# Optimization experiments

Hardware: AMD Instinct MI355X
Metric: run time of the kernel (lower is better)

The kernel has to match this reference:

```python
import jax, jax.numpy as jnp
import numpy as np

N = 100000      # nodes
E = 1600000     # nnz of precomputed A^K (avg degree 16)
D = 64          # in_feats
C = 64          # n_classes
LN_EPS = 1e-5


def setup_inputs() -> dict:
    key = jax.random.key(0)
    ks = jax.random.split(key, 8)
    feat = jax.random.normal(ks[0], (N, D), dtype=jnp.float32)
    feat_ori = jax.random.normal(ks[1], (N, D), dtype=jnp.float32)
    row = jax.random.randint(ks[2], (E,), 0, N)
    col = jax.random.randint(ks[3], (E,), 0, N)
    adj_vals = jax.random.uniform(ks[4], (E,), dtype=jnp.float32)
    # Linear params (xavier_uniform weight, zero bias)
    limit = float(np.sqrt(6.0 / (D + C)))
    W = jax.random.uniform(ks[5], (C, D), dtype=jnp.float32, minval=-limit, maxval=limit)
    b = jnp.zeros((C,), dtype=jnp.float32)
    # LayerNorm params
    gamma = jnp.ones((C,), dtype=jnp.float32)
    beta = jnp.zeros((C,), dtype=jnp.float32)
    return {"feat": feat, "feat_ori": feat_ori, "row": row, "col": col,
            "adj_vals": adj_vals, "W": W, "b": b, "gamma": gamma, "beta": beta}


def reference(feat, feat_ori, row, col, adj_vals, W, b, gamma, beta):
    # NOTE: in the source, h = (1-alpha)*feat + alpha*feat_ori is dead code
    # (immediately overwritten by the SpMM of raw feat), so it is omitted.
    # SpMM: h[i] = sum_{e: row[e]=i} adj_vals[e] * feat[col[e]]   -> [N, D]
    msgs = adj_vals[:, None] * feat[col]            # [E, D] gather + scale
    h = jax.ops.segment_sum(msgs, row, num_segments=N)  # [N, D] scatter-add
    # Dense Linear: [N, D] @ [D, C] + [C]
    h = jnp.einsum('nd,cd->nc', h, W) + b
    # LayerNorm over last dim
    mu = jnp.mean(h, axis=-1, keepdims=True)
    var = jnp.mean(jnp.square(h - mu), axis=-1, keepdims=True)
    h = (h - mu) * jax.lax.rsqrt(var + LN_EPS) * gamma + beta
    return h
```

## Files before the change

### kernel.cpp

```cpp
#include <hip/hip_runtime.h>


typedef unsigned int u32;
typedef unsigned short u16;
typedef unsigned long long u64;
#define RFL(x) __builtin_amdgcn_readfirstlane(x)

#define NBLKC 64
#define MAXBK 2048
#define CAP 1280

__device__ __forceinline__ float bf2f(u16 v) {
    return __uint_as_float((u32)v << 16);
}
__device__ __forceinline__ u16 f2bf(float f) {
    u32 b = __float_as_uint(f);
    return (u16)((b + 0x7FFFu + ((b >> 16) & 1u)) >> 16);
}

__global__ __launch_bounds__(256) void k_bhist(const int* __restrict__ row,
                                               u32* __restrict__ hist2d,
                                               int E, int NBK, int CH) {
    __shared__ u32 cnt[MAXBK];
    int tid = threadIdx.x;
    for (int i = tid; i < NBK; i += 256) cnt[i] = 0;
    __syncthreads();
    int e0 = blockIdx.x * CH;
    int e1 = e0 + CH; if (e1 > E) e1 = E;
    int ev = e1 & ~3;
    for (int i = e0 + tid * 4; i < ev; i += 1024) {
        int4 r = *reinterpret_cast<const int4*>(&row[i]);
        atomicAdd(&cnt[(u32)r.x >> 6], 1u);
        atomicAdd(&cnt[(u32)r.y >> 6], 1u);
        atomicAdd(&cnt[(u32)r.z >> 6], 1u);
        atomicAdd(&cnt[(u32)r.w >> 6], 1u);
    }
    { int i = ev + tid; if (i < e1) atomicAdd(&cnt[(u32)row[i] >> 6], 1u); }
    __syncthreads();
    u32* dst = hist2d + (size_t)blockIdx.x * NBK;
    for (int i = tid; i < NBK; i += 256) dst[i] = cnt[i];
}

__device__ __forceinline__ u32 blk_scan256(u32 v, u32* wsum, u32& total) {
    int lane = threadIdx.x & 63, wid = threadIdx.x >> 6;
    u32 incl = v;
#pragma unroll
    for (int o = 1; o < 64; o <<= 1) {
        u32 u = __shfl_up(incl, o);
        if (lane >= o) incl += u;
    }
    if (lane == 63) wsum[wid] = incl;
    __syncthreads();
    u32 woff = 0;
    for (int w = 0; w < wid; ++w) woff += wsum[w];
    total = wsum[0] + wsum[1] + wsum[2] + wsum[3];
    __syncthreads();
    return woff + incl - v;
}

__global__ __launch_bounds__(256) void k_bscan(u32* __restrict__ hist2d,
                                               u32* __restrict__ btot,
                                               int NBLK, int NBK) {
    __shared__ u32 wsum[4];
    int bkt = blockIdx.x;
    u32 carry = 0;
    for (int r = 0; r < NBLK; r += 256) {
        int blk = r + threadIdx.x;
        u32 v = (blk < NBLK) ? hist2d[(size_t)blk * NBK + bkt] : 0;
        u32 tot;
        u32 ex = blk_scan256(v, wsum, tot);
        if (blk < NBLK) hist2d[(size_t)blk * NBK + bkt] = ex + carry;
        carry += tot;
    }
    if (threadIdx.x == 0) btot[bkt] = carry;
}

__global__ __launch_bounds__(256) void k_scanb2(const u32* __restrict__ btot,
                                                u32* __restrict__ bbase,
                                                int NBK, int E) {
    __shared__ u32 wsum[4];
    u32 carry = 0;
    for (int r = 0; r < NBK; r += 256) {
        int i = r + threadIdx.x;
        u32 v = (i < NBK) ? btot[i] : 0;
        u32 tot;
        u32 ex = blk_scan256(v, wsum, tot);
        if (i < NBK) bbase[i] = ex + carry;
        carry += tot;
    }
    if (threadIdx.x == 0) bbase[NBK] = (u32)E;
}

__global__ __launch_bounds__(256) void k_scatgemm(
    const int* __restrict__ row, const int* __restrict__ col,
    const float* __restrict__ vals, const u32* __restrict__ hist2d,
    const u32* __restrict__ bbase, u64* __restrict__ epair1,
    const float* __restrict__ feat, const float* __restrict__ W,
    u16* __restrict__ G, int E, int N, int NBK, int NBLK, int CH)
{
    __shared__ __align__(16) u32 smem[4096];
    int tid = threadIdx.x;
    if ((int)blockIdx.x < NBLK) {
        u32* lbase = smem;
        u32* lcnt  = smem + NBK;
        int blk = blockIdx.x;
        const u32* hrow = hist2d + (size_t)blk * NBK;
        for (int i = tid; i < NBK; i += 256) {
            lbase[i] = bbase[i] + hrow[i];
            lcnt[i] = 0;
        }
        __syncthreads();
        int e0 = blk * CH;
        int e1 = e0 + CH; if (e1 > E) e1 = E;
        int ev = e1 & ~3;
        for (int i = e0 + tid * 4; i < ev; i += 1024) {
            int4 r = *reinterpret_cast<const int4*>(&row[i]);
            int4 c = *reinterpret_cast<const int4*>(&col[i]);
            float4 v = *reinterpret_cast<const float4*>(&vals[i]);
            u32 k0 = (u32)r.x >> 6, k1 = (u32)r.y >> 6;
            u32 k2 = (u32)r.z >> 6, k3 = (u32)r.w >> 6;
            u32 q0 = atomicAdd(&lcnt[k0], 1u);
            u32 q1 = atomicAdd(&lcnt[k1], 1u);
            u32 q2 = atomicAdd(&lcnt[k2], 1u);
            u32 q3 = atomicAdd(&lcnt[k3], 1u);
            epair1[lbase[k0] + q0] = (u64)((u32)c.x | (((u32)r.x & 63u) << 26))
                                   | ((u64)__float_as_uint(v.x) << 32);
            epair1[lbase[k1] + q1] = (u64)((u32)c.y | (((u32)r.y & 63u) << 26))
                                   | ((u64)__float_as_uint(v.y) << 32);
            epair1[lbase[k2] + q2] = (u64)((u32)c.z | (((u32)r.z & 63u) << 26))
                                   | ((u64)__float_as_uint(v.z) << 32);
            epair1[lbase[k3] + q3] = (u64)((u32)c.w | (((u32)r.w & 63u) << 26))
                                   | ((u64)__float_as_uint(v.w) << 32);
        }
        {
            int i = ev + tid;
            if (i < e1) {
                u32 r = (u32)row[i];
                u32 k = r >> 6;
                u32 q = atomicAdd(&lcnt[k], 1u);
                epair1[lbase[k] + q] = (u64)((u32)col[i] | ((r & 63u) << 26))
                                     | ((u64)__float_as_uint(vals[i]) << 32);
            }
        }
    } else {
        float* fs = (float*)smem;
        int lane = tid & 63, wid = tid >> 6;
        int n0 = ((int)blockIdx.x - NBLK) * 64;
        int valid = N - n0; if (valid > 64) valid = 64;
        int elems = valid * 64;
        for (int idx = tid * 4; idx < elems; idx += 1024)
            *reinterpret_cast<float4*>(&fs[idx]) =
                *reinterpret_cast<const float4*>(&feat[(size_t)n0 * 64 + idx]);
        float wr[64];
#pragma unroll
        for (int d4 = 0; d4 < 16; ++d4) {
            float4 w4 = *reinterpret_cast<const float4*>(&W[lane * 64 + d4 * 4]);
            wr[d4 * 4 + 0] = w4.x; wr[d4 * 4 + 1] = w4.y;
            wr[d4 * 4 + 2] = w4.z; wr[d4 * 4 + 3] = w4.w;
        }
        __syncthreads();
        for (int j = 0; j < 16; ++j) {
            int r = wid * 16 + j;
            if (r >= valid) break;
            float oa[4] = {0.f, 0.f, 0.f, 0.f};
#pragma unroll
            for (int d4 = 0; d4 < 16; ++d4) {
                float4 h4 = *reinterpret_cast<const float4*>(&fs[r * 64 + d4 * 4]);
                oa[d4 & 3] = fmaf(h4.x, wr[d4 * 4 + 0],
                            fmaf(h4.y, wr[d4 * 4 + 1],
                            fmaf(h4.z, wr[d4 * 4 + 2],
                            fmaf(h4.w, wr[d4 * 4 + 3], oa[d4 & 3]))));
            }
            G[(size_t)(n0 + r) * 64 + lane] = f2bf((oa[0] + oa[1]) + (oa[2] + oa[3]));
        }
    }
}

__global__ __launch_bounds__(256) void k_node2(
    const u16* __restrict__ G, const u64* __restrict__ epair1,
    const u32* __restrict__ bbase, const float* __restrict__ bias,
    const float* __restrict__ gamma, const float* __restrict__ beta,
    float* __restrict__ out, int N)
{
    __shared__ u64 sp[CAP];
    __shared__ u32 cnt[64], base[64], cnt2[32];
    int tid = threadIdx.x, lane = tid & 63, wid = tid >> 6;
    int bkt  = blockIdx.x >> 1;
    int half = blockIdx.x & 1;
    if (tid < 64) cnt[tid] = 0;
    if (tid < 32) cnt2[tid] = 0;
    __syncthreads();
    int s = RFL((int)bbase[bkt]);
    int t = RFL((int)bbase[bkt + 1]);

    const u32* meta1 = (const u32*)epair1;
    for (int i = s + tid; i < t; i += 256)
        atomicAdd(&cnt[meta1[2 * (size_t)i] >> 26], 1u);
    __syncthreads();
    if (tid < 64) {
        u32 v = cnt[tid];
        u32 incl = v;
#pragma unroll
        for (int o = 1; o < 64; o <<= 1) {
            u32 u = __shfl_up(incl, o);
            if (tid >= o) incl += u;
        }
        base[tid] = incl - v;
    }
    __syncthreads();
    int r0 = half << 5;
    int myoff = base[r0];
    int myend = (half ? (t - s) : base[32]);
    int myedges = myend - myoff;
    bool fits = (myedges <= CAP);

    if (fits) {
        for (int i = s + tid; i < t; i += 256) {
            u64 p = epair1[i];
            u32 mm = (u32)p;
            u32 r = mm >> 26;
            if ((int)(r >> 5) == half) {
                u32 rank = atomicAdd(&cnt2[r & 31u], 1u);
                sp[base[r] - myoff + rank] =
                    (p & 0xFFFFFFFF00000000ull) | (u64)(mm & 0x03FFFFFFu);
            }
        }
    }
    __syncthreads();

    int rbase = (bkt << 6) + r0;
    for (int j = 0; j < 8; ++j) {
        int rr = (wid << 3) + j;
        int r = r0 + rr;
        int n = rbase + rr;
        if (n >= N) break;
        float acc0 = 0.f, acc1 = 0.f;
        if (fits) {
            int e0 = base[r] - myoff, e1 = e0 + cnt[r];
            int i = e0;
            for (; i + 8 <= e1; i += 8) {
                u64 p0 = sp[i],     p1 = sp[i + 1];
                u64 p2 = sp[i + 2], p3 = sp[i + 3];
                u64 p4 = sp[i + 4], p5 = sp[i + 5];
                u64 p6 = sp[i + 6], p7 = sp[i + 7];
                u32 c0 = RFL((u32)p0), b0 = RFL((u32)(p0 >> 32));
                u32 c1 = RFL((u32)p1), b1 = RFL((u32)(p1 >> 32));
                u32 c2 = RFL((u32)p2), b2 = RFL((u32)(p2 >> 32));
                u32 c3 = RFL((u32)p3), b3 = RFL((u32)(p3 >> 32));
                u32 c4 = RFL((u32)p4), b4 = RFL((u32)(p4 >> 32));
                u32 c5 = RFL((u32)p5), b5 = RFL((u32)(p5 >> 32));
                u32 c6 = RFL((u32)p6), b6 = RFL((u32)(p6 >> 32));
                u32 c7 = RFL((u32)p7), b7 = RFL((u32)(p7 >> 32));
                float g0 = bf2f(G[((size_t)c0 << 6) | lane]);
                float g1 = bf2f(G[((size_t)c1 << 6) | lane]);
                float g2 = bf2f(G[((size_t)c2 << 6) | lane]);
                float g3 = bf2f(G[((size_t)c3 << 6) | lane]);
                float g4 = bf2f(G[((size_t)c4 << 6) | lane]);
                float g5 = bf2f(G[((size_t)c5 << 6) | lane]);
                float g6 = bf2f(G[((size_t)c6 << 6) | lane]);
                float g7 = bf2f(G[((size_t)c7 << 6) | lane]);
                acc0 = fmaf(__uint_as_float(b0), g0, acc0);
                acc1 = fmaf(__uint_as_float(b1), g1, acc1);
                acc0 = fmaf(__uint_as_float(b2), g2, acc0);
                acc1 = fmaf(__uint_as_float(b3), g3, acc1);
                acc0 = fmaf(__uint_as_float(b4), g4, acc0);
                acc1 = fmaf(__uint_as_float(b5), g5, acc1);
                acc0 = fmaf(__uint_as_float(b6), g6, acc0);
                acc1 = fmaf(__uint_as_float(b7), g7, acc1);
            }
            for (; i < e1; ++i) {
                u64 p = sp[i];
                u32 c = RFL((u32)p), b = RFL((u32)(p >> 32));
                acc0 = fmaf(__uint_as_float(b), bf2f(G[((size_t)c << 6) | lane]), acc0);
            }
        } else {
            for (int i = s; i < t; ++i) {
                u64 p = epair1[i];
                u32 mm = RFL((u32)p);
                if ((int)(mm >> 26) == r) {
                    u32 b = RFL((u32)(p >> 32));
                    acc0 = fmaf(__uint_as_float(b),
                                bf2f(G[((size_t)(mm & 0x03FFFFFFu) << 6) | lane]), acc0);
                }
            }
        }
        float o = acc0 + acc1 + bias[lane];

        float ssum = o;
#pragma unroll
        for (int off = 32; off; off >>= 1) ssum += __shfl_xor(ssum, off);
        float mu = ssum * 0.015625f;
        float dv = o - mu;
        float vs = dv * dv;
#pragma unroll
        for (int off = 32; off; off >>= 1) vs += __shfl_xor(vs, off);
        float inv = rsqrtf(vs * 0.015625f + 1e-5f);
        out[((size_t)n << 6) + lane] = dv * inv * gamma[lane] + beta[lane];
    }
}

extern "C" void kernel_launch(void* const* d_in, const int* in_sizes, int n_in,
                              void* d_out, int out_size, void* d_ws, size_t ws_size,
                              hipStream_t stream) {
    const float* feat  = (const float*)d_in[0];
    const int*   row   = (const int*)d_in[2];
    const int*   col   = (const int*)d_in[3];
    const float* vals  = (const float*)d_in[4];
    const float* W     = (const float*)d_in[5];
    const float* bias  = (const float*)d_in[6];
    const float* gamma = (const float*)d_in[7];
    const float* beta  = (const float*)d_in[8];
    float* out = (float*)d_out;

    const int D = 64;
    int N = in_sizes[0] / D;
    int E = in_sizes[2];

    int NBK  = (N + 63) / 64;
    int NBLK = NBLKC;
    int CH   = (((E + NBLK - 1) / NBLK) + 3) & ~3;
    int NG   = (N + 63) / 64;

    char* ws = (char*)d_ws;
    u16*   G      = (u16*)ws;
    size_t off1   = (((size_t)N * 128) + 255) & ~(size_t)255;
    u64*   epair1 = (u64*)(ws + off1);
    size_t off2   = off1 + (((size_t)E * 8 + 255) & ~(size_t)255);
    u32*   hist2d = (u32*)(ws + off2);
    size_t off3   = off2 + (((size_t)NBLK * NBK * 4 + 255) & ~(size_t)255);
    u32*   btot   = (u32*)(ws + off3);
    u32*   bbase  = btot + NBK;

    k_bhist   <<<NBLK, 256, 0, stream>>>(row, hist2d, E, NBK, CH);
    k_bscan   <<<NBK, 256, 0, stream>>>(hist2d, btot, NBLK, NBK);
    k_scanb2  <<<1, 256, 0, stream>>>(btot, bbase, NBK, E);
    k_scatgemm<<<NBLK + NG, 256, 0, stream>>>(row, col, vals, hist2d, bbase,
                                              epair1, feat, W, G,
                                              E, N, NBK, NBLK, CH);
    k_node2   <<<NBK * 2, 256, 0, stream>>>(G, epair1, bbase, bias, gamma,
                                            beta, out, N);
}
```

Before: 134.2 us.

## Split fused scatter/GEMM kernel and widen scatter to 128 blocks of 1024 threads

Splits the combined scatter+GEMM kernel into a dedicated bucket-scatter kernel and a separate feature-transform GEMM kernel, launched back to back. The edge chunk count doubles to 128, and each scatter block now runs 1024 threads, so many more waves place edges into buckets. This targets the scatter phase, which ran on only 64 blocks of 256 threads. In exchange it adds a kernel launch, serializes the GEMM after the scatter instead of overlapping them in one grid, and doubles the histogram/scan work over blocks.

Result: slower. 143.4 us (+6.8%).

```diff
diff --git a/kernel.cpp b/kernel.cpp
--- a/kernel.cpp
+++ b/kernel.cpp
@@ -6,7 +6,7 @@
 typedef unsigned long long u64;
 #define RFL(x) __builtin_amdgcn_readfirstlane(x)
 
-#define NBLKC 64
+#define NBLKC 128
 #define MAXBK 2048
 #define CAP 1280
 
@@ -91,88 +91,88 @@
     if (threadIdx.x == 0) bbase[NBK] = (u32)E;
 }
 
-__global__ __launch_bounds__(256) void k_scatgemm(
+__global__ __launch_bounds__(1024) void k_scat(
     const int* __restrict__ row, const int* __restrict__ col,
     const float* __restrict__ vals, const u32* __restrict__ hist2d,
     const u32* __restrict__ bbase, u64* __restrict__ epair1,
-    const float* __restrict__ feat, const float* __restrict__ W,
-    u16* __restrict__ G, int E, int N, int NBK, int NBLK, int CH)
+    int E, int NBK, int CH)
 {
-    __shared__ __align__(16) u32 smem[4096];
+    __shared__ u32 lbase[MAXBK];
+    __shared__ u32 lcnt[MAXBK];
     int tid = threadIdx.x;
-    if ((int)blockIdx.x < NBLK) {
-        u32* lbase = smem;
-        u32* lcnt  = smem + NBK;
-        int blk = blockIdx.x;
-        const u32* hrow = hist2d + (size_t)blk * NBK;
-        for (int i = tid; i < NBK; i += 256) {
-            lbase[i] = bbase[i] + hrow[i];
-            lcnt[i] = 0;
-        }
-        __syncthreads();
-        int e0 = blk * CH;
-        int e1 = e0 + CH; if (e1 > E) e1 = E;
-        int ev = e1 & ~3;
-        for (int i = e0 + tid * 4; i < ev; i += 1024) {
-            int4 r = *reinterpret_cast<const int4*>(&row[i]);
-            int4 c = *reinterpret_cast<const int4*>(&col[i]);
-            float4 v = *reinterpret_cast<const float4*>(&vals[i]);
-            u32 k0 = (u32)r.x >> 6, k1 = (u32)r.y >> 6;
-            u32 k2 = (u32)r.z >> 6, k3 = (u32)r.w >> 6;
-            u32 q0 = atomicAdd(&lcnt[k0], 1u);
-            u32 q1 = atomicAdd(&lcnt[k1], 1u);
-            u32 q2 = atomicAdd(&lcnt[k2], 1u);
-            u32 q3 = atomicAdd(&lcnt[k3], 1u);
-            epair1[lbase[k0] + q0] = (u64)((u32)c.x | (((u32)r.x & 63u) << 26))
-                                   | ((u64)__float_as_uint(v.x) << 32);
-            epair1[lbase[k1] + q1] = (u64)((u32)c.y | (((u32)r.y & 63u) << 26))
-                                   | ((u64)__float_as_uint(v.y) << 32);
-            epair1[lbase[k2] + q2] = (u64)((u32)c.z | (((u32)r.z & 63u) << 26))
-                                   | ((u64)__float_as_uint(v.z) << 32);
-            epair1[lbase[k3] + q3] = (u64)((u32)c.w | (((u32)r.w & 63u) << 26))
-                                   | ((u64)__float_as_uint(v.w) << 32);
-        }
-        {
-            int i = ev + tid;
-            if (i < e1) {
-                u32 r = (u32)row[i];
-                u32 k = r >> 6;
-                u32 q = atomicAdd(&lcnt[k], 1u);
-                epair1[lbase[k] + q] = (u64)((u32)col[i] | ((r & 63u) << 26))
-                                     | ((u64)__float_as_uint(vals[i]) << 32);
-            }
-        }
-    } else {
-        float* fs = (float*)smem;
-        int lane = tid & 63, wid = tid >> 6;
-        int n0 = ((int)blockIdx.x - NBLK) * 64;
-        int valid = N - n0; if (valid > 64) valid = 64;
-        int elems = valid * 64;
-        for (int idx = tid * 4; idx < elems; idx += 1024)
-            *reinterpret_cast<float4*>(&fs[idx]) =
-                *reinterpret_cast<const float4*>(&feat[(size_t)n0 * 64 + idx]);
-        float wr[64];
+    int blk = blockIdx.x;
+    const u32* hrow = hist2d + (size_t)blk * NBK;
+    for (int i = tid; i < NBK; i += 1024) {
+        lbase[i] = bbase[i] + hrow[i];
+        lcnt[i] = 0;
+    }
+    __syncthreads();
+    int e0 = blk * CH;
+    int e1 = e0 + CH; if (e1 > E) e1 = E;
+    int ev = e1 & ~3;
+    for (int i = e0 + tid * 4; i < ev; i += 4096) {
+        int4 r = *reinterpret_cast<const int4*>(&row[i]);
+        int4 c = *reinterpret_cast<const int4*>(&col[i]);
+        float4 v = *reinterpret_cast<const float4*>(&vals[i]);
+        u32 k0 = (u32)r.x >> 6, k1 = (u32)r.y >> 6;
+        u32 k2 = (u32)r.z >> 6, k3 = (u32)r.w >> 6;
+        u32 q0 = atomicAdd(&lcnt[k0], 1u);
+        u32 q1 = atomicAdd(&lcnt[k1], 1u);
+        u32 q2 = atomicAdd(&lcnt[k2], 1u);
+        u32 q3 = atomicAdd(&lcnt[k3], 1u);
+        epair1[lbase[k0] + q0] = (u64)((u32)c.x | (((u32)r.x & 63u) << 26))
+                               | ((u64)__float_as_uint(v.x) << 32);
+        epair1[lbase[k1] + q1] = (u64)((u32)c.y | (((u32)r.y & 63u) << 26))
+                               | ((u64)__float_as_uint(v.y) << 32);
+        epair1[lbase[k2] + q2] = (u64)((u32)c.z | (((u32)r.z & 63u) << 26))
+                               | ((u64)__float_as_uint(v.z) << 32);
+        epair1[lbase[k3] + q3] = (u64)((u32)c.w | (((u32)r.w & 63u) << 26))
+                               | ((u64)__float_as_uint(v.w) << 32);
+    }
+    {
+        int i = ev + tid;
+        if (i < e1) {
+            u32 r = (u32)row[i];
+            u32 k = r >> 6;
+            u32 q = atomicAdd(&lcnt[k], 1u);
+            epair1[lbase[k] + q] = (u64)((u32)col[i] | ((r & 63u) << 26))
+                                 | ((u64)__float_as_uint(vals[i]) << 32);
+        }
+    }
+}
+
+__global__ __launch_bounds__(256) void k_gemm(const float* __restrict__ feat,
+                                              const float* __restrict__ W,
+                                              u16* __restrict__ G, int N) {
+    __shared__ float fs[4096];
+    int lane = threadIdx.x & 63, wid = threadIdx.x >> 6;
+    int n0 = blockIdx.x * 64;
+    int valid = N - n0; if (valid > 64) valid = 64;
+    int elems = valid * 64;
+    for (int idx = threadIdx.x * 4; idx < elems; idx += 1024)
+        *reinterpret_cast<float4*>(&fs[idx]) =
+            *reinterpret_cast<const float4*>(&feat[(size_t)n0 * 64 + idx]);
+    float wr[64];
+#pragma unroll
+    for (int d4 = 0; d4 < 16; ++d4) {
+        float4 w4 = *reinterpret_cast<const float4*>(&W[lane * 64 + d4 * 4]);
+        wr[d4 * 4 + 0] = w4.x; wr[d4 * 4 + 1] = w4.y;
+        wr[d4 * 4 + 2] = w4.z; wr[d4 * 4 + 3] = w4.w;
+    }
+    __syncthreads();
+    for (int j = 0; j < 16; ++j) {
+        int r = wid * 16 + j;
+        if (r >= valid) break;
+        float oa[4] = {0.f, 0.f, 0.f, 0.f};
 #pragma unroll
         for (int d4 = 0; d4 < 16; ++d4) {
-            float4 w4 = *reinterpret_cast<const float4*>(&W[lane * 64 + d4 * 4]);
-            wr[d4 * 4 + 0] = w4.x; wr[d4 * 4 + 1] = w4.y;
-            wr[d4 * 4 + 2] = w4.z; wr[d4 * 4 + 3] = w4.w;
-        }
-        __syncthreads();
-        for (int j = 0; j < 16; ++j) {
-            int r = wid * 16 + j;
-            if (r >= valid) break;
-            float oa[4] = {0.f, 0.f, 0.f, 0.f};
-#pragma unroll
-            for (int d4 = 0; d4 < 16; ++d4) {
-                float4 h4 = *reinterpret_cast<const float4*>(&fs[r * 64 + d4 * 4]);
-                oa[d4 & 3] = fmaf(h4.x, wr[d4 * 4 + 0],
-                            fmaf(h4.y, wr[d4 * 4 + 1],
-                            fmaf(h4.z, wr[d4 * 4 + 2],
-                            fmaf(h4.w, wr[d4 * 4 + 3], oa[d4 & 3]))));
-            }
-            G[(size_t)(n0 + r) * 64 + lane] = f2bf((oa[0] + oa[1]) + (oa[2] + oa[3]));
-        }
+            float4 h4 = *reinterpret_cast<const float4*>(&fs[r * 64 + d4 * 4]);
+            oa[d4 & 3] = fmaf(h4.x, wr[d4 * 4 + 0],
+                        fmaf(h4.y, wr[d4 * 4 + 1],
+                        fmaf(h4.z, wr[d4 * 4 + 2],
+                        fmaf(h4.w, wr[d4 * 4 + 3], oa[d4 & 3]))));
+        }
+        G[(size_t)(n0 + r) * 64 + lane] = f2bf((oa[0] + oa[1]) + (oa[2] + oa[3]));
     }
 }
 
@@ -331,12 +331,12 @@
     u32*   btot   = (u32*)(ws + off3);
     u32*   bbase  = btot + NBK;
 
-    k_bhist   <<<NBLK, 256, 0, stream>>>(row, hist2d, E, NBK, CH);
-    k_bscan   <<<NBK, 256, 0, stream>>>(hist2d, btot, NBLK, NBK);
-    k_scanb2  <<<1, 256, 0, stream>>>(btot, bbase, NBK, E);
-    k_scatgemm<<<NBLK + NG, 256, 0, stream>>>(row, col, vals, hist2d, bbase,
-                                              epair1, feat, W, G,
-                                              E, N, NBK, NBLK, CH);
-    k_node2   <<<NBK * 2, 256, 0, stream>>>(G, epair1, bbase, bias, gamma,
-                                            beta, out, N);
-}
+    k_bhist <<<NBLK, 256, 0, stream>>>(row, hist2d, E, NBK, CH);
+    k_bscan <<<NBK, 256, 0, stream>>>(hist2d, btot, NBLK, NBK);
+    k_scanb2<<<1, 256, 0, stream>>>(btot, bbase, NBK, E);
+    k_scat  <<<NBLK, 1024, 0, stream>>>(row, col, vals, hist2d, bbase,
+                                        epair1, E, NBK, CH);
+    k_gemm  <<<NG, 256, 0, stream>>>(feat, W, G, N);
+    k_node2 <<<NBK * 2, 256, 0, stream>>>(G, epair1, bbase, bias, gamma,
+                                          beta, out, N);
+}
```
